# Performance work log

Hardware: AMD Instinct MI355X
Metric: run time of the kernel (lower is better)

Reference implementation:

```python
import jax, jax.numpy as jnp
import numpy as np

SQ, B, NH, HD = 2048, 2, 16, 128  # seq, batch, heads, head_dim


def setup_inputs() -> dict:
    key = jax.random.key(0)
    kq, kk, kv = jax.random.split(key, 3)
    shape = (SQ, B, NH, HD)
    return {
        "query": jax.random.normal(kq, shape, dtype=jnp.float32),
        "key": jax.random.normal(kk, shape, dtype=jnp.float32),
        "value": jax.random.normal(kv, shape, dtype=jnp.float32),
        "attention_mask": jnp.ones((B, 1, SQ, SQ), dtype=bool),
    }


def reference(query, key, value, attention_mask):
    # query/key/value: [s, b, n, h]
    sq, b, n_heads, hn = query.shape
    norm_factor = jnp.sqrt(jnp.asarray(hn, query.dtype))
    # QK^T -> [b, n, sq, sk]
    scores = jnp.einsum("sbnh,tbnh->bnst", query, key) / norm_factor
    probs = jax.nn.softmax(scores, axis=-1, where=attention_mask)
    # PV -> [s, b, n, h]  (dropout is identity at p=0.0 / eval)
    context = jnp.einsum("bnst,tbnh->sbnh", probs, value)
    return context.reshape(sq, b, n_heads * hn)
```

## Files before the change

kernel.cpp:

```cpp
#include <hip/hip_runtime.h>
#include <hip/hip_bf16.h>
#include <math.h>


#define SQ 2048
#define NBH 32
#define HD 128
#define RSTRIDE 4096
#define BQ 256
#define BK 64
#define NKT (SQ / BK)
#define HELEMS (SQ * HD)
#define SCALE_LOG2E 0.12751879523499918f

typedef __attribute__((ext_vector_type(4)))  float f32x4;
typedef __attribute__((ext_vector_type(16))) float f32x16;
typedef __attribute__((ext_vector_type(4)))  short s16x4;
typedef __attribute__((ext_vector_type(8)))  short s16x8;

#define MFMA32(a, b, c) __builtin_amdgcn_mfma_f32_32x32x16_bf16((a), (b), (c), 0, 0, 0)

__device__ __forceinline__ short f2bf(float f) {
    __hip_bfloat16 h = __float2bfloat16(f);
    return __builtin_bit_cast(short, h);
}
__device__ __forceinline__ unsigned pk2(float lo, float hi) {
    unsigned r;
    asm("v_cvt_pk_bf16_f32 %0, %1, %2" : "=v"(r) : "v"(lo), "v"(hi));
    return r;
}

__device__ __forceinline__ void stage16(const void* g, void* l) {
    __builtin_amdgcn_global_load_lds(
        (const __attribute__((address_space(1))) unsigned int*)g,
        (__attribute__((address_space(3))) unsigned int*)l, 16, 0, 0);
}

__global__ __launch_bounds__(256) void prep_qk(const float* __restrict__ Q,
                                               const float* __restrict__ K,
                                               short* __restrict__ wq,
                                               short* __restrict__ wk) {
    const int id = blockIdx.x * 256 + threadIdx.x;
    const int bh = id >> 15;
    const int s  = (id >> 4) & 2047;
    const int c  = id & 15;
    const size_t outoff = (size_t)bh * HELEMS + (size_t)s * HD + c * 8;
    {
        const float* src = Q + (size_t)s * RSTRIDE + bh * HD + c * 8;
        f32x4 a = *(const f32x4*)src;
        f32x4 b = *(const f32x4*)(src + 4);
        s16x8 f;
        #pragma unroll
        for (int j = 0; j < 4; ++j) {
            f[j]     = f2bf(a[j] * SCALE_LOG2E);
            f[4 + j] = f2bf(b[j] * SCALE_LOG2E);
        }
        *(s16x8*)(wq + outoff) = f;
    }
    {
        const int cl = c ^ (s & 7);
        const float* src = K + (size_t)s * RSTRIDE + bh * HD + cl * 8;
        f32x4 a = *(const f32x4*)src;
        f32x4 b = *(const f32x4*)(src + 4);
        s16x8 f;
        #pragma unroll
        for (int j = 0; j < 4; ++j) { f[j] = f2bf(a[j]); f[4 + j] = f2bf(b[j]); }
        *(s16x8*)(wk + outoff) = f;
    }
}

__global__ __launch_bounds__(256) void prep_v(const float* __restrict__ V,
                                              short* __restrict__ wv) {
    const int kt = blockIdx.x;
    const int bh = blockIdx.y;
    const int tid = threadIdx.x;
    __shared__ short L[64 * 132];

    #pragma unroll
    for (int it = 0; it < 8; ++it) {
        const int id = it * 256 + tid;
        const int row = id >> 5, p = id & 31;
        f32x4 a = *(const f32x4*)(V + (size_t)(kt * BK + row) * RSTRIDE + bh * HD + p * 4);
        s16x4 f;
        #pragma unroll
        for (int j = 0; j < 4; ++j) f[j] = f2bf(a[j]);
        *(s16x4*)&L[row * 132 + p * 4] = f;
    }
    __syncthreads();
    #pragma unroll
    for (int it = 0; it < 4; ++it) {
        const int id = it * 256 + tid;
        const int dim = id >> 3, c = id & 7;
        const int klb = (c ^ (dim & 7)) * 8;
        s16x8 f;
        #pragma unroll
        for (int j = 0; j < 8; ++j) f[j] = L[(klb + j) * 132 + dim];
        *(s16x8*)(wv + (size_t)bh * HELEMS + (size_t)dim * SQ + kt * BK + c * 8) = f;
    }
}

__global__ __launch_bounds__(512) void fa_fwd10(const short* __restrict__ Qb,
                                                const short* __restrict__ Kb,
                                                const short* __restrict__ Vb,
                                                float* __restrict__ O) {
    const int id  = blockIdx.x;
    const int xcd = id & 7;
    const int s8  = id >> 3;
    const int bh  = xcd * 4 + (s8 >> 3);
    const int qt  = s8 & 7;

    const int tid  = threadIdx.x;
    const int w    = tid >> 6;
    const int lane = tid & 63;
    const int l32  = lane & 31;
    const int hi   = lane >> 5;

    __shared__ short Kt[4][BK * HD];
    __shared__ short Vt[4][HD * BK];

    const size_t hb = (size_t)bh * HELEMS;
    const int q = qt * BQ + w * 32 + l32;

    s16x8 qf[8];
    {
        const short* qp = Qb + hb + (size_t)q * HD + hi * 8;
        #pragma unroll
        for (int kd = 0; kd < 8; ++kd) qf[kd] = *(const s16x8*)(qp + kd * 16);
    }

    f32x16 acc[4];
    #pragma unroll
    for (int db = 0; db < 4; ++db)
        #pragma unroll
        for (int i = 0; i < 16; ++i) acc[db][i] = 0.0f;
    float l = 0.0f;

    auto STAGE = [&](int kt, int buf) {
        if (w < 4) {
            const short* kg = Kb + hb + (size_t)kt * (BK * HD) + w * 2048 + lane * 8;
            short* ld = &Kt[buf][w * 2048 + lane * 8];
            #pragma unroll
            for (int j = 0; j < 4; ++j)
                stage16(kg + j * 512, ld + j * 512);
        } else {
            const int w4 = w - 4;
            #pragma unroll
            for (int j = 0; j < 4; ++j) {
                const int dim = w4 * 32 + j * 8 + (lane >> 3);
                const short* vg = Vb + hb + (size_t)dim * SQ + kt * BK + (lane & 7) * 8;
                stage16(vg, &Vt[buf][(w4 * 32 + j * 8) * BK + lane * 8]);
            }
        }
    };

    auto BODY = [&](int bufi) {
        f32x16 sc[2];
        const short* Kb_ = Kt[bufi];
        __builtin_amdgcn_s_setprio(1);
        #pragma unroll
        for (int kb = 0; kb < 2; ++kb) {
            #pragma unroll
            for (int i = 0; i < 16; ++i) sc[kb][i] = 0.0f;
            const int key = kb * 32 + l32;
            #pragma unroll
            for (int kd = 0; kd < 8; ++kd) {
                const int elem = key * HD + (((kd << 1) | hi) ^ (key & 7)) * 8;
                s16x8 kf = *(const s16x8*)&Kb_[elem];
                sc[kb] = MFMA32(kf, qf[kd], sc[kb]);
            }
        }
        __builtin_amdgcn_s_setprio(0);

        float lsp0 = 0.f, lsp1 = 0.f, lsp2 = 0.f, lsp3 = 0.f;
        #pragma unroll
        for (int kb = 0; kb < 2; ++kb)
            #pragma unroll
            for (int r = 0; r < 16; r += 4) {
                float p0 = exp2f(sc[kb][r + 0]);
                float p1 = exp2f(sc[kb][r + 1]);
                float p2 = exp2f(sc[kb][r + 2]);
                float p3 = exp2f(sc[kb][r + 3]);
                sc[kb][r + 0] = p0; sc[kb][r + 1] = p1;
                sc[kb][r + 2] = p2; sc[kb][r + 3] = p3;
                lsp0 += p0; lsp1 += p1; lsp2 += p2; lsp3 += p3;
            }
        l += (lsp0 + lsp1) + (lsp2 + lsp3);

        s16x8 pa[4];
        #pragma unroll
        for (int ks = 0; ks < 4; ++ks) {
            const int kb = ks >> 1;
            const int j  = (2 * ks) & 3, j2 = (2 * ks + 1) & 3;
            unsigned a0 = pk2(sc[kb][4 * j + 0],  sc[kb][4 * j + 1]);
            unsigned a1 = pk2(sc[kb][4 * j + 2],  sc[kb][4 * j + 3]);
            unsigned b0 = pk2(sc[kb][4 * j2 + 0], sc[kb][4 * j2 + 1]);
            unsigned b1 = pk2(sc[kb][4 * j2 + 2], sc[kb][4 * j2 + 3]);
#if __has_builtin(__builtin_amdgcn_permlane32_swap)
            auto r0 = __builtin_amdgcn_permlane32_swap(a0, b0, false, false);
            auto r1 = __builtin_amdgcn_permlane32_swap(a1, b1, false, false);
            union { unsigned u[4]; s16x8 v; } P;
            P.u[0] = r0[0]; P.u[1] = r1[0]; P.u[2] = r0[1]; P.u[3] = r1[1];
#else
            const unsigned s0 = __shfl_xor(hi ? a0 : b0, 32, 64);
            const unsigned s1 = __shfl_xor(hi ? a1 : b1, 32, 64);
            union { unsigned u[4]; s16x8 v; } P;
            P.u[0] = hi ? s0 : a0; P.u[1] = hi ? s1 : a1;
            P.u[2] = hi ? b0 : s0; P.u[3] = hi ? b1 : s1;
#endif
            pa[ks] = P.v;
        }

        const short* Vb_ = Vt[bufi];
        __builtin_amdgcn_s_setprio(1);
        #pragma unroll
        for (int db = 0; db < 4; ++db) {
            const int dim = db * 32 + l32;
            #pragma unroll
            for (int ks = 0; ks < 4; ++ks) {
                const int elem = dim * BK + ((((ks << 1) | hi) ^ (dim & 7)) << 3);
                s16x8 vf = *(const s16x8*)&Vb_[elem];
                acc[db] = MFMA32(vf, pa[ks], acc[db]);
            }
        }
        __builtin_amdgcn_s_setprio(0);
    };

    STAGE(0, 0);
    STAGE(1, 1);
    __syncthreads();

    #pragma unroll 1
    for (int i = 0; i < NKT / 2; ++i) {
        const int t0 = 2 * i;
        if (t0 + 2 < NKT) STAGE(t0 + 2, (t0 + 2) & 3);
        if (t0 + 3 < NKT) STAGE(t0 + 3, (t0 + 3) & 3);
        BODY(t0 & 3);
        BODY((t0 + 1) & 3);
        __syncthreads();
    }

    const float lf = l + __shfl_xor(l, 32, 64);
    const float invl = 1.0f / lf;
    float* op = O + (size_t)q * RSTRIDE + bh * HD;
    #pragma unroll
    for (int db = 0; db < 4; ++db)
        #pragma unroll
        for (int j = 0; j < 4; ++j) {
            f32x4 o;
            #pragma unroll
            for (int r = 0; r < 4; ++r) o[r] = acc[db][4 * j + r] * invl;
            *(f32x4*)(op + db * 32 + j * 8 + hi * 4) = o;
        }
}

__global__ __launch_bounds__(256) void fa_fwd_legacy(const float* __restrict__ Q,
                                                     const float* __restrict__ K,
                                                     const float* __restrict__ V,
                                                     float* __restrict__ O) {
    const int qt   = blockIdx.x;
    const int bh   = blockIdx.y;
    const int tid  = threadIdx.x;
    const int w    = tid >> 6;
    const int lane = tid & 63;
    const int l16  = lane & 15;
    const int lg   = lane >> 4;

    __shared__ short Kt[BK * HD];
    __shared__ short Vt[HD * BK];
    __shared__ short Pl[4][16 * 72];

    const int headoff = bh * HD;
    s16x8 qf[4];
    {
        const int qrow = qt * 64 + w * 16 + l16;
        const float* qp = Q + (size_t)qrow * RSTRIDE + headoff + lg * 8;
        #pragma unroll
        for (int ks = 0; ks < 4; ++ks) {
            f32x4 a = *(const f32x4*)(qp + ks * 32);
            f32x4 b = *(const f32x4*)(qp + ks * 32 + 4);
            s16x8 f;
            #pragma unroll
            for (int j = 0; j < 4; ++j) {
                f[j]     = f2bf(a[j] * SCALE_LOG2E);
                f[4 + j] = f2bf(b[j] * SCALE_LOG2E);
            }
            qf[ks] = f;
        }
    }
    f32x4 acc[8];
    #pragma unroll
    for (int i = 0; i < 8; ++i)
        #pragma unroll
        for (int j = 0; j < 4; ++j) acc[i][j] = 0.0f;
    float mrow[4], lrow[4];
    #pragma unroll
    for (int r = 0; r < 4; ++r) { mrow[r] = -INFINITY; lrow[r] = 0.0f; }
    const int skey = tid >> 2;
    const int sdc  = tid & 3;
    const int va   = tid >> 3;
    const int vdc  = tid & 7;

    for (int kt = 0; kt < NKT; ++kt) {
        __syncthreads();
        {
            const float* kp = K + (size_t)(kt * BK + skey) * RSTRIDE + headoff;
            #pragma unroll
            for (int c = 0; c < 4; ++c) {
                const int d0 = c * 32 + sdc * 8;
                f32x4 a = *(const f32x4*)(kp + d0);
                f32x4 b = *(const f32x4*)(kp + d0 + 4);
                s16x8 f;
                #pragma unroll
                for (int j = 0; j < 4; ++j) { f[j] = f2bf(a[j]); f[4 + j] = f2bf(b[j]); }
                const int elem = (skey * HD + d0) ^ ((skey & 7) << 3);
                *(s16x8*)&Kt[elem] = f;
            }
        }
        {
            const float* vp0 = V + (size_t)(kt * BK + va * 2) * RSTRIDE + headoff;
            const float* vp1 = vp0 + RSTRIDE;
            #pragma unroll
            for (int c = 0; c < 4; ++c) {
                const int d0 = c * 32 + vdc * 4;
                f32x4 a0 = *(const f32x4*)(vp0 + d0);
                f32x4 a1 = *(const f32x4*)(vp1 + d0);
                #pragma unroll
                for (int j = 0; j < 4; ++j) {
                    const int dim = d0 + j;
                    const int s = (dim ^ (dim >> 3)) & 7;
                    const int elem = (dim * BK + va * 2) ^ (s << 3);
                    union { short u[2]; int i; } pr;
                    pr.u[0] = f2bf(a0[j]);
                    pr.u[1] = f2bf(a1[j]);
                    *(int*)&Vt[elem] = pr.i;
                }
            }
        }
        __syncthreads();
        f32x4 sc[4];
        #pragma unroll
        for (int t = 0; t < 4; ++t) {
            #pragma unroll
            for (int j = 0; j < 4; ++j) sc[t][j] = 0.0f;
            const int key = t * 16 + l16;
            #pragma unroll
            for (int ks = 0; ks < 4; ++ks) {
                const int elem = (key * HD + ks * 32 + lg * 8) ^ ((key & 7) << 3);
                s16x8 kf = *(const s16x8*)&Kt[elem];
                sc[t] = __builtin_amdgcn_mfma_f32_16x16x32_bf16(qf[ks], kf, sc[t], 0, 0, 0);
            }
        }
        float alpha[4];
        #pragma unroll
        for (int r = 0; r < 4; ++r) {
            float m0 = fmaxf(fmaxf(sc[0][r], sc[1][r]), fmaxf(sc[2][r], sc[3][r]));
            #pragma unroll
            for (int d = 1; d < 16; d <<= 1) m0 = fmaxf(m0, __shfl_xor(m0, d, 64));
            const float mnew = fmaxf(mrow[r], m0);
            alpha[r] = exp2f(mrow[r] - mnew);
            mrow[r] = mnew;
        }
        float rsum[4] = {0.f, 0.f, 0.f, 0.f};
        #pragma unroll
        for (int t = 0; t < 4; ++t)
            #pragma unroll
            for (int r = 0; r < 4; ++r) {
                const float p = exp2f(sc[t][r] - mrow[r]);
                sc[t][r] = p;
                rsum[r] += p;
            }
        #pragma unroll
        for (int r = 0; r < 4; ++r) {
            #pragma unroll
            for (int d = 1; d < 16; d <<= 1) rsum[r] += __shfl_xor(rsum[r], d, 64);
            lrow[r] = lrow[r] * alpha[r] + rsum[r];
        }
        #pragma unroll
        for (int ct = 0; ct < 8; ++ct)
            #pragma unroll
            for (int r = 0; r < 4; ++r) acc[ct][r] *= alpha[r];
        #pragma unroll
        for (int t = 0; t < 4; ++t)
            #pragma unroll
            for (int r = 0; r < 4; ++r)
                Pl[w][(lg * 4 + r) * 72 + t * 16 + l16] = f2bf(sc[t][r]);
        s16x8 pf[2];
        #pragma unroll
        for (int ks = 0; ks < 2; ++ks)
            pf[ks] = *(const s16x8*)&Pl[w][l16 * 72 + ks * 32 + lg * 8];
        #pragma unroll
        for (int ct = 0; ct < 8; ++ct) {
            const int dim = ct * 16 + l16;
            const int s = (dim ^ (dim >> 3)) & 7;
            #pragma unroll
            for (int ks = 0; ks < 2; ++ks) {
                const int elem = (dim * BK + ks * 32 + lg * 8) ^ (s << 3);
                s16x8 vf = *(const s16x8*)&Vt[elem];
                acc[ct] = __builtin_amdgcn_mfma_f32_16x16x32_bf16(pf[ks], vf, acc[ct], 0, 0, 0);
            }
        }
    }
    float inv_l[4];
    #pragma unroll
    for (int r = 0; r < 4; ++r) inv_l[r] = 1.0f / lrow[r];
    const int orow0 = qt * 64 + w * 16;
    #pragma unroll
    for (int ct = 0; ct < 8; ++ct) {
        const int col = ct * 16 + l16;
        #pragma unroll
        for (int r = 0; r < 4; ++r) {
            const int row = orow0 + lg * 4 + r;
            O[(size_t)row * RSTRIDE + headoff + col] = acc[ct][r] * inv_l[r];
        }
    }
}

extern "C" void kernel_launch(void* const* d_in, const int* in_sizes, int n_in,
                              void* d_out, int out_size, void* d_ws, size_t ws_size,
                              hipStream_t stream) {
    const float* Q = (const float*)d_in[0];
    const float* K = (const float*)d_in[1];
    const float* V = (const float*)d_in[2];
    float* O = (float*)d_out;

    const size_t need = (size_t)3 * NBH * HELEMS * sizeof(short);
    if (ws_size >= need) {
        short* wq = (short*)d_ws;
        short* wk = wq + (size_t)NBH * HELEMS;
        short* wv = wk + (size_t)NBH * HELEMS;
        prep_qk<<<4096, 256, 0, stream>>>(Q, K, wq, wk);
        prep_v<<<dim3(NKT, NBH), 256, 0, stream>>>(V, wv);
        fa_fwd10<<<(SQ / BQ) * NBH, 512, 0, stream>>>(wq, wk, wv, O);
    } else {
        fa_fwd_legacy<<<dim3(SQ / 64, NBH), 256, 0, stream>>>(Q, K, V, O);
    }
}
```

Measured before the change: 122.5 us.

## Split key range across two warp groups per block with LDS reduction

```diff
diff --git a/kernel.cpp b/kernel.cpp
--- a/kernel.cpp
+++ b/kernel.cpp
@@ -99,10 +99,10 @@
     }
 }
 
-__global__ __launch_bounds__(512) void fa_fwd10(const short* __restrict__ Qb,
-                                                const short* __restrict__ Kb,
-                                                const short* __restrict__ Vb,
-                                                float* __restrict__ O) {
+__global__ __launch_bounds__(1024) void fa_fwd11(const short* __restrict__ Qb,
+                                                 const short* __restrict__ Kb,
+                                                 const short* __restrict__ Vb,
+                                                 float* __restrict__ O) {
     const int id  = blockIdx.x;
     const int xcd = id & 7;
     const int s8  = id >> 3;
@@ -111,15 +111,17 @@
 
     const int tid  = threadIdx.x;
     const int w    = tid >> 6;
+    const int g    = w >> 3;
+    const int w8   = w & 7;
     const int lane = tid & 63;
     const int l32  = lane & 31;
     const int hi   = lane >> 5;
 
-    __shared__ short Kt[4][BK * HD];
-    __shared__ short Vt[4][HD * BK];
+    __shared__ short Kt[2][2][BK * HD];
+    __shared__ short Vt[2][2][BK * HD];
 
     const size_t hb = (size_t)bh * HELEMS;
-    const int q = qt * BQ + w * 32 + l32;
+    const int q = qt * BQ + w8 * 32 + l32;
 
     s16x8 qf[8];
     {
@@ -136,26 +138,37 @@
     float l = 0.0f;
 
     auto STAGE = [&](int kt, int buf) {
-        if (w < 4) {
-            const short* kg = Kb + hb + (size_t)kt * (BK * HD) + w * 2048 + lane * 8;
-            short* ld = &Kt[buf][w * 2048 + lane * 8];
+        if (w8 < 4) {
+            const short* kg = Kb + hb + (size_t)kt * (BK * HD) + w8 * 2048 + lane * 8;
+            short* ld = &Kt[g][buf][w8 * 2048 + lane * 8];
             #pragma unroll
             for (int j = 0; j < 4; ++j)
                 stage16(kg + j * 512, ld + j * 512);
         } else {
-            const int w4 = w - 4;
+            const int w4 = w8 - 4;
             #pragma unroll
             for (int j = 0; j < 4; ++j) {
                 const int dim = w4 * 32 + j * 8 + (lane >> 3);
                 const short* vg = Vb + hb + (size_t)dim * SQ + kt * BK + (lane & 7) * 8;
-                stage16(vg, &Vt[buf][(w4 * 32 + j * 8) * BK + lane * 8]);
+                stage16(vg, &Vt[g][buf][(w4 * 32 + j * 8) * BK + lane * 8]);
             }
         }
     };
 
-    auto BODY = [&](int bufi) {
+    const int nkt = NKT / 2;
+    const int kt0 = g * nkt;
+
+    STAGE(kt0, 0);
+    __syncthreads();
+    int buf = 0;
+
+    #pragma unroll 1
+    for (int t = 0; t < nkt; ++t) {
+        const int kt = kt0 + t;
+        if (t + 1 < nkt) STAGE(kt + 1, buf ^ 1);
+
         f32x16 sc[2];
-        const short* Kb_ = Kt[bufi];
+        const short* Kb_ = Kt[g][buf];
         __builtin_amdgcn_s_setprio(1);
         #pragma unroll
         for (int kb = 0; kb < 2; ++kb) {
@@ -210,7 +223,7 @@
             pa[ks] = P.v;
         }
 
-        const short* Vb_ = Vt[bufi];
+        const short* Vb_ = Vt[g][buf];
         __builtin_amdgcn_s_setprio(1);
         #pragma unroll
         for (int db = 0; db < 4; ++db) {
@@ -223,34 +236,57 @@
             }
         }
         __builtin_amdgcn_s_setprio(0);
-    };
-
-    STAGE(0, 0);
-    STAGE(1, 1);
+
+        __syncthreads();
+        buf ^= 1;
+    }
+
+    const float lf = l + __shfl_xor(l, 32, 64);
+
+    float* Lm = (float*)&Kt[0][0][0];
+    if (g == 1 && hi == 0) Lm[w8 * 32 + l32] = lf;
     __syncthreads();
-
+    const float ltot = lf + ((g == 0) ? Lm[w8 * 32 + l32] : 0.0f);
+
+    float* Am = (float*)&Vt[0][0][0];
     #pragma unroll 1
-    for (int i = 0; i < NKT / 2; ++i) {
-        const int t0 = 2 * i;
-        if (t0 + 2 < NKT) STAGE(t0 + 2, (t0 + 2) & 3);
-        if (t0 + 3 < NKT) STAGE(t0 + 3, (t0 + 3) & 3);
-        BODY(t0 & 3);
-        BODY((t0 + 1) & 3);
+    for (int db = 0; db < 4; ++db) {
         __syncthreads();
-    }
-
-    const float lf = l + __shfl_xor(l, 32, 64);
-    const float invl = 1.0f / lf;
-    float* op = O + (size_t)q * RSTRIDE + bh * HD;
-    #pragma unroll
-    for (int db = 0; db < 4; ++db)
-        #pragma unroll
-        for (int j = 0; j < 4; ++j) {
-            f32x4 o;
-            #pragma unroll
-            for (int r = 0; r < 4; ++r) o[r] = acc[db][4 * j + r] * invl;
-            *(f32x4*)(op + db * 32 + j * 8 + hi * 4) = o;
-        }
+        if (g == 1) {
+            float* row = Am + (w8 * 32 + l32) * 36;
+            #pragma unroll
+            for (int j = 0; j < 4; ++j) {
+                f32x4 v;
+                #pragma unroll
+                for (int r = 0; r < 4; ++r) v[r] = acc[db][4 * j + r];
+                *(f32x4*)(row + j * 8 + hi * 4) = v;
+            }
+        }
+        __syncthreads();
+        if (g == 0) {
+            const float* row = Am + (w8 * 32 + l32) * 36;
+            #pragma unroll
+            for (int j = 0; j < 4; ++j) {
+                f32x4 v = *(const f32x4*)(row + j * 8 + hi * 4);
+                #pragma unroll
+                for (int r = 0; r < 4; ++r) acc[db][4 * j + r] += v[r];
+            }
+        }
+    }
+
+    if (g == 0) {
+        const float invl = 1.0f / ltot;
+        float* op = O + (size_t)q * RSTRIDE + bh * HD;
+        #pragma unroll
+        for (int db = 0; db < 4; ++db)
+            #pragma unroll
+            for (int j = 0; j < 4; ++j) {
+                f32x4 o;
+                #pragma unroll
+                for (int r = 0; r < 4; ++r) o[r] = acc[db][4 * j + r] * invl;
+                *(f32x4*)(op + db * 32 + j * 8 + hi * 4) = o;
+            }
+    }
 }
 
 __global__ __launch_bounds__(256) void fa_fwd_legacy(const float* __restrict__ Q,
@@ -430,7 +466,7 @@
         short* wv = wk + (size_t)NBH * HELEMS;
         prep_qk<<<4096, 256, 0, stream>>>(Q, K, wq, wk);
         prep_v<<<dim3(NKT, NBH), 256, 0, stream>>>(V, wv);
-        fa_fwd10<<<(SQ / BQ) * NBH, 512, 0, stream>>>(wq, wk, wv, O);
+        fa_fwd11<<<(SQ / BQ) * NBH, 1024, 0, stream>>>(wq, wk, wv, O);
     } else {
         fa_fwd_legacy<<<dim3(SQ / 64, NBH), 256, 0, stream>>>(Q, K, V, O);
     }
```

After: 369.6 us. 202% more time.
